# Optimization experiments

Measured on AMD Instinct MI355X. Metric: run time of the kernel, lower is better.

## Reference

```python
import jax, jax.numpy as jnp
import numpy as np

P, D, NF, NR, ND, EF, ER = 512, 128, 50000, 50000, 100000, 400000, 400000
BASELINE = 6.0


def setup_inputs() -> dict:
    key = jax.random.key(0)
    ctr = [0]
    def nk():
        ctr[0] += 1
        return jax.random.fold_in(key, ctr[0])
    def nrm(shape, scale=1.0):
        return jax.random.normal(nk(), shape, dtype=jnp.float32) * scale
    def uni(shape):
        return jax.random.uniform(nk(), shape, dtype=jnp.float32)
    def lin(fi, fo):
        return nrm((fi, fo), fi ** -0.5), jnp.zeros((fo,), jnp.float32)
    inp = {}
    inp['target_features'] = nrm((P,))
    inp['form_features'] = nrm((NF, P))
    inp['role_features'] = nrm((NR, P))
    inp['form_binds_y'] = BASELINE + nrm((EF,))
    inp['form_binds_w'] = uni((EF,))
    inp['role_binds_y'] = BASELINE + nrm((ER,))
    inp['role_binds_w'] = uni((ER,))
    inp['form_diff_w'] = uni((NF,)) + 0.01
    inp['role_diff_w'] = uni((NR,)) + 0.01
    inp['trust_vector'] = uni((3,))
    inp['drug_features'] = nrm((ND, D))
    inp['form_w1'], inp['form_b1'] = lin(P, P); inp['form_a1'] = jnp.full((1,), 0.25, jnp.float32)
    inp['form_w2'], inp['form_b2'] = lin(P, P)
    inp['role_w1'], inp['role_b1'] = lin(P, P); inp['role_a1'] = jnp.full((1,), 0.25, jnp.float32)
    inp['role_w2'], inp['role_b2'] = lin(P, P)
    inp['q_w'], inp['q_b'] = lin(P, D)
    inp['k_w'], inp['k_b'] = lin(D, D)
    inp['v_w'], inp['v_b'] = lin(D, D)
    inp['layer_emb'] = nrm((2, 16))
    inp['attn_w1'], inp['attn_b1'] = lin(2 * P + 16, 128)
    inp['attn_w2'], inp['attn_b2'] = lin(128, 64)
    inp['attn_w3'], inp['attn_b3'] = lin(64, 1)
    inp['mix_w1'], inp['mix_b1'] = lin(2 * D + 3, 64); inp['mix_a'] = jnp.full((1,), 0.25, jnp.float32)
    inp['mix_w2'], inp['mix_b2'] = lin(64, 2)
    inp['int_w1'], inp['int_b1'] = lin(D, P); inp['int_a'] = jnp.full((1,), 0.25, jnp.float32)
    inp['int_w2'], inp['int_b2'] = lin(P, P)
    inp['norm_w'] = jnp.ones((P,), jnp.float32)
    inp['norm_b'] = jnp.zeros((P,), jnp.float32)
    inp['delta_gate'] = jnp.float32(0.5)
    inp['form_neighbors'] = jnp.arange(NF, dtype=jnp.int32)
    inp['role_neighbors'] = jnp.arange(NR, dtype=jnp.int32)
    inp['form_binds_src'] = jax.random.randint(nk(), (EF,), 0, NF, dtype=jnp.int32)
    inp['form_binds_dst'] = jax.random.randint(nk(), (EF,), 0, ND, dtype=jnp.int32)
    inp['role_binds_src'] = jax.random.randint(nk(), (ER,), 0, NR, dtype=jnp.int32)
    inp['role_binds_dst'] = jax.random.randint(nk(), (ER,), 0, ND, dtype=jnp.int32)
    return inp


def _prelu(x, a):
    return jnp.where(x >= 0, x, a * x)


def _mlp2(x, w1, b1, a, w2, b2):
    return _prelu(x @ w1 + b1, a) @ w2 + b2


def _ln(x, w=None, b=None, eps=1e-5):
    m = jnp.mean(x, -1, keepdims=True)
    v = jnp.mean((x - m) ** 2, -1, keepdims=True)
    y = (x - m) * jax.lax.rsqrt(v + eps)
    return y if w is None else y * w + b


def _pref(z, nid, src, dst, y, w, drugs, q_w, q_b, k_w, k_b, v_w, v_b):
    # segment-softmax attention over (neighbor protein -> drug) bipartite edges
    N = nid.shape[0]
    order = jnp.argsort(nid)
    s = nid[order]
    pos = jnp.searchsorted(s, src)
    clip = jnp.minimum(pos, N - 1)
    valid = (pos < N) & (s[clip] == src)
    seg = jnp.where(valid, order[clip], N)  # invalid edges -> dump segment N
    q = z @ q_w + q_b                       # [D]
    d = drugs[dst]                          # [E, D] gather
    k = d @ k_w + k_b
    v = (d @ v_w + v_b) * ((y - BASELINE) * w)[:, None]
    logits = (k @ q) / (k.shape[-1] ** 0.5)
    mx = jax.ops.segment_max(logits, seg, num_segments=N + 1)
    mx = jnp.where(jnp.isfinite(mx), mx, 0.0)
    ex = jnp.where(valid, jnp.exp(logits - mx[seg]), 0.0)
    den = jax.ops.segment_sum(ex, seg, num_segments=N + 1) + 1e-12
    attn = ex / den[seg]
    return jax.ops.segment_sum(v * attn[:, None], seg, num_segments=N + 1)[:N]


def _attn_logits(z, zn, lemb, w1, b1, w2, b2, w3, b3):
    N = zn.shape[0]
    x = jnp.concatenate([jnp.broadcast_to(z, (N, z.shape[0])), zn,
                         jnp.broadcast_to(lemb, (N, lemb.shape[0]))], axis=-1)
    h = jax.nn.leaky_relu(x @ w1 + b1, 0.2)
    h = jax.nn.leaky_relu(h @ w2 + b2, 0.2)
    return (h @ w3 + b3)[:, 0]


def _core(fl, form_neighbors, role_neighbors, form_binds_src, form_binds_dst, role_binds_src, role_binds_dst):
    (target_features, form_features, role_features, form_binds_y, form_binds_w,
     role_binds_y, role_binds_w, form_diff_w, role_diff_w, trust_vector, drug_features,
     form_w1, form_b1, form_a1, form_w2, form_b2,
     role_w1, role_b1, role_a1, role_w2, role_b2,
     q_w, q_b, k_w, k_b, v_w, v_b, layer_emb,
     attn_w1, attn_b1, attn_w2, attn_b2, attn_w3, attn_b3,
     mix_w1, mix_b1, mix_a, mix_w2, mix_b2,
     int_w1, int_b1, int_a, int_w2, int_b2,
     norm_w, norm_b, delta_gate) = fl
    z_form = _mlp2(target_features, form_w1, form_b1, form_a1, form_w2, form_b2)
    z_role = _mlp2(target_features, role_w1, role_b1, role_a1, role_w2, role_b2)
    z = 0.5 * (z_form + z_role)
    form_feats = _mlp2(form_features, form_w1, form_b1, form_a1, form_w2, form_b2)
    role_feats = _mlp2(role_features, role_w1, role_b1, role_a1, role_w2, role_b2)
    form_msgs = _pref(z, form_neighbors, form_binds_src, form_binds_dst, form_binds_y, form_binds_w, drug_features, q_w, q_b, k_w, k_b, v_w, v_b)
    role_msgs = _pref(z, role_neighbors, role_binds_src, role_binds_dst, role_binds_y, role_binds_w, drug_features, q_w, q_b, k_w, k_b, v_w, v_b)
    form_logits = _attn_logits(z, form_feats, layer_emb[0], attn_w1, attn_b1, attn_w2, attn_b2, attn_w3, attn_b3)
    role_logits = _attn_logits(z, role_feats, layer_emb[1], attn_w1, attn_b1, attn_w2, attn_b2, attn_w3, attn_b3)
    form_attn = jax.nn.softmax(form_logits + jnp.log(jnp.maximum(form_diff_w, 1e-12)))
    role_attn = jax.nn.softmax(role_logits + jnp.log(jnp.maximum(role_diff_w, 1e-12)))
    v_form = form_attn @ form_msgs
    v_role = role_attn @ role_msgs
    mixer_in = jnp.concatenate([v_form, v_role, trust_vector])
    lw = jax.nn.softmax(_mlp2(mixer_in, mix_w1, mix_b1, mix_a, mix_w2, mix_b2))
    w_form, w_role = lw[0], lw[1]
    v_prior = w_form * v_form + w_role * v_role
    form_delta = form_attn @ (z[None, :] - form_feats)
    role_delta = role_attn @ (z[None, :] - role_feats)
    delta_raw = w_form * form_delta + w_role * role_delta
    delta_mean = delta_gate * _ln(delta_raw)
    z_refined = _ln(z + _mlp2(v_prior, int_w1, int_b1, int_a, int_w2, int_b2), norm_w, norm_b)
    return z_refined, v_prior, delta_mean


def reference(target_features, form_features, role_features, form_binds_y, form_binds_w, role_binds_y, role_binds_w, form_diff_w, role_diff_w, trust_vector, drug_features, form_w1, form_b1, form_a1, form_w2, form_b2, role_w1, role_b1, role_a1, role_w2, role_b2, q_w, q_b, k_w, k_b, v_w, v_b, layer_emb, attn_w1, attn_b1, attn_w2, attn_b2, attn_w3, attn_b3, mix_w1, mix_b1, mix_a, mix_w2, mix_b2, int_w1, int_b1, int_a, int_w2, int_b2, norm_w, norm_b, delta_gate, form_neighbors, role_neighbors, form_binds_src, form_binds_dst, role_binds_src, role_binds_dst):
    fl = (target_features, form_features, role_features, form_binds_y, form_binds_w,
          role_binds_y, role_binds_w, form_diff_w, role_diff_w, trust_vector, drug_features,
          form_w1, form_b1, form_a1, form_w2, form_b2,
          role_w1, role_b1, role_a1, role_w2, role_b2,
          q_w, q_b, k_w, k_b, v_w, v_b, layer_emb,
          attn_w1, attn_b1, attn_w2, attn_b2, attn_w3, attn_b3,
          mix_w1, mix_b1, mix_a, mix_w2, mix_b2,
          int_w1, int_b1, int_a, int_w2, int_b2,
          norm_w, norm_b, delta_gate)
    return _core(fl, form_neighbors, role_neighbors, form_binds_src, form_binds_dst, role_binds_src, role_binds_dst)
```

## Files before the change

kernel.cpp:

```cpp
#include <hip/hip_runtime.h>

#define NFN 50000
#define NDR 100000
#define NE  400000

__device__ __forceinline__ float bf2f(unsigned short u) {
    return __uint_as_float(((unsigned)u) << 16);
}
__device__ __forceinline__ unsigned short f2bf(float f) {
    unsigned u = __float_as_uint(f);
    unsigned r = 0x7FFFu + ((u >> 16) & 1u);
    return (unsigned short)((u + r) >> 16);
}

typedef __attribute__((ext_vector_type(8))) short bf16x8;
typedef __attribute__((ext_vector_type(4))) float f32x4;

struct KArgs {
    const float *tf, *ff, *rf, *fby, *fbw, *rby, *rbw, *fdw, *rdw, *trust, *drugs;
    const float *fw1, *fb1, *fa1, *fw2, *fb2, *rw1, *rb1, *ra1, *rw2, *rb2;
    const float *qw, *qb, *kw, *kb, *vw, *vb, *lemb;
    const float *aw1, *ab1, *aw2, *ab2, *aw3, *ab3;
    const float *mw1, *mb1, *ma, *mw2, *mb2;
    const float *iw1, *ib1, *ia, *iw2, *ib2;
    const float *nw, *nb, *dgate;
    const int *fsrc, *fdst, *rsrc, *rdst;
    float *shf, *shr;
    float *svf, *svr;
    float *gdenf, *gdenr;
    float *edenf, *edenr;
    float *cdf, *cdr;
    float *hraw;
    float *zraw;
    float *qraw;
    float *b1f, *b1r;
    float *sfr;
    float *o2raw;
    float *qk, *c0, *pe;
    unsigned short *w1tf, *w1tr;
    unsigned short *w2atf, *w2atr;
    unsigned short *aw2t;
    float *nexf, *nexr;
    unsigned short *H;
    unsigned short *Xb;
    float *hi;
    float *wfwr;
    float *out;
};

__global__ __launch_bounds__(512) void kA(KArgs A) {
    const int b = blockIdx.x;
    const int side = b >> 5, chunk = b & 31;
    const int tt = threadIdx.x;
    const float* w1 = side ? A.rw1 : A.fw1;
    float acc = 0.f;
    const int i0 = chunk * 16;
#pragma unroll
    for (int k = 0; k < 16; k++) {
        int i = i0 + k;
        acc = fmaf(A.tf[i], w1[(size_t)i * 512 + tt], acc);
    }
    atomicAdd(&A.hraw[side * 512 + tt], acc);
}

__global__ __launch_bounds__(512) void kB(KArgs A) {
    const int b = blockIdx.x;
    const int side = b >> 4, chunk = b & 15;
    const int tt = threadIdx.x;
    const float* w2 = side ? A.rw2 : A.fw2;
    const float* b1 = side ? A.rb1 : A.fb1;
    const float aa = (side ? A.ra1 : A.fa1)[0];
    float acc = 0.f;
    const int i0 = chunk * 32;
    for (int k = 0; k < 32; k++) {
        int i = i0 + k;
        float h = A.hraw[side * 512 + i] + b1[i];
        h = h >= 0.f ? h : aa * h;
        acc = fmaf(h, w2[(size_t)i * 512 + tt], acc);
    }
    if (b == 0) acc += A.fb2[tt] + A.rb2[tt];
    atomicAdd(&A.zraw[tt], acc);
}

__global__ __launch_bounds__(512) void kC1(KArgs A) {
    const int b = blockIdx.x;
    const int t = threadIdx.x;
    const int j = t & 127, isub = t >> 7;
    if (b < 8) {
        const int i0 = b * 64 + isub * 16;
        float acc = 0.f;
        for (int k = 0; k < 16; k++) {
            int i = i0 + k;
            acc = fmaf(0.5f * A.zraw[i], A.qw[(size_t)i * 128 + j], acc);
        }
        atomicAdd(&A.qraw[j], acc);
        if (b == 0 && t < 128) atomicAdd(&A.qraw[t], A.qb[t]);
    } else if (b < 16) {
        const int chunk = b - 8;
        const int i0 = chunk * 64 + isub * 16;
        float acc = 0.f;
        for (int k = 0; k < 16; k++) {
            int i = i0 + k;
            acc = fmaf(0.5f * A.zraw[i], A.aw1[(size_t)i * 128 + j], acc);
            acc = fmaf(A.fb2[i], A.aw1[(size_t)(512 + i) * 128 + j], acc);
        }
        atomicAdd(&A.b1f[j], acc);
        if (b == 8 && t < 128) {
            float c = A.ab1[t];
            for (int l = 0; l < 16; l++) c = fmaf(A.lemb[l], A.aw1[(size_t)(1024 + l) * 128 + t], c);
            atomicAdd(&A.b1f[t], c);
        }
    } else {
        const int chunk = b - 16;
        const int i0 = chunk * 64 + isub * 16;
        float acc = 0.f;
        for (int k = 0; k < 16; k++) {
            int i = i0 + k;
            acc = fmaf(0.5f * A.zraw[i], A.aw1[(size_t)i * 128 + j], acc);
            acc = fmaf(A.rb2[i], A.aw1[(size_t)(512 + i) * 128 + j], acc);
        }
        atomicAdd(&A.b1r[j], acc);
        if (b == 16 && t < 128) {
            float c = A.ab1[t];
            for (int l = 0; l < 16; l++) c = fmaf(A.lemb[16 + l], A.aw1[(size_t)(1024 + l) * 128 + t], c);
            atomicAdd(&A.b1r[t], c);
        }
    }
}

__global__ __launch_bounds__(256) void kC2(KArgs A) {
    const int t = threadIdx.x;
    __shared__ float sq[128];
    if (t < 128) sq[t] = A.qraw[t];
    __syncthreads();
    if (t < 128) {
        float s = 0.f;
        for (int j = 0; j < 128; j++) s = fmaf(A.kw[t * 128 + j], sq[j], s);
        A.qk[t] = s;
    } else if (t == 128) {
        float c = 0.f;
        for (int j = 0; j < 128; j++) c = fmaf(A.kb[j], sq[j], c);
        A.c0[0] = c;
    }
}

__global__ __launch_bounds__(256) void k_cvtX(const float* __restrict__ in,
                                              unsigned short* __restrict__ out, int n4) {
    int idx = blockIdx.x * 256 + threadIdx.x;
    const int stride = gridDim.x * 256;
    for (; idx < n4; idx += stride) {
        float4 v = ((const float4*)in)[idx];
        uint2 o;
        o.x = (unsigned)f2bf(v.x) | ((unsigned)f2bf(v.y) << 16);
        o.y = (unsigned)f2bf(v.z) | ((unsigned)f2bf(v.w) << 16);
        ((uint2*)out)[idx] = o;
    }
}

__global__ __launch_bounds__(512) void k_cvtW(KArgs A) {
    const int side = blockIdx.x >> 9;
    const int k = blockIdx.x & 511;
    const int n = threadIdx.x;
    const float* w1 = side ? A.rw1 : A.fw1;
    unsigned short* o = side ? A.w1tr : A.w1tf;
    o[(size_t)n * 512 + k] = f2bf(w1[k * 512 + n]);
}

__global__ __launch_bounds__(128) void k_cvtA2(KArgs A) {
    const int j = blockIdx.x;
    const int i = threadIdx.x;
    A.aw2t[j * 128 + i] = f2bf(A.aw2[i * 64 + j]);
}

__global__ __launch_bounds__(128) void k_w2a(KArgs A) {
    const int side = blockIdx.x >> 9;
    const int i = blockIdx.x & 511;
    const int j = threadIdx.x;
    const float* w2 = side ? A.rw2 : A.fw2;
    unsigned short* outp = side ? A.w2atr : A.w2atf;
    float s = 0.f;
    for (int k = 0; k < 512; k++)
        s = fmaf(w2[i * 512 + k], A.aw1[(size_t)(512 + k) * 128 + j], s);
    outp[(size_t)j * 512 + i] = f2bf(s);
}

__global__ __launch_bounds__(256, 2)
void mfma_gemm(const unsigned short* __restrict__ Ab, const unsigned short* __restrict__ Bt,
               const float* __restrict__ bias, const float* __restrict__ actp,
               unsigned short* __restrict__ Cv, int M, int N, int K, int NT) {
    __shared__ __align__(16) unsigned short Abuf[2][128 * 32];
    __shared__ __align__(16) unsigned short Bbuf[2][128 * 32];
    const int t = threadIdx.x;
    const int lane = t & 63, wv = t >> 6;
    int bid = blockIdx.x;
    if (NT > 1) {
        const int nwg = gridDim.x;
        const int q = nwg >> 3, r = nwg & 7;
        const int xcd = bid & 7, lx = bid >> 3;
        bid = (xcd < r ? xcd * (q + 1) : r * (q + 1) + (xcd - r) * q) + lx;
    }
    const int m0 = (bid / NT) * 128, n0 = (bid % NT) * 128;
    const int wm = (wv >> 1) * 64, wn = (wv & 1) * 64;
    const int lm = lane & 15, ko = lane >> 4;

    f32x4 acc[4][4];
#pragma unroll
    for (int i = 0; i < 4; i++)
#pragma unroll
        for (int j = 0; j < 4; j++) acc[i][j] = (f32x4){0.f, 0.f, 0.f, 0.f};

    const int nk = K >> 5;

    auto stage = [&](int buf, int k0) {
#pragma unroll
        for (int ii = 0; ii < 2; ii++) {
            const int inst = wv * 2 + ii;
            const int rl = inst * 16 + (lane >> 2);
            const int sl = (lane & 3) ^ ((rl >> 1) & 3);
            int ar = m0 + rl; if (ar >= M) ar = M - 1;
            __builtin_amdgcn_global_load_lds(
                (const __attribute__((address_space(1))) void*)(Ab + (size_t)ar * K + k0 + sl * 8),
                (__attribute__((address_space(3))) void*)(&Abuf[buf][inst * 512]), 16, 0, 0);
            __builtin_amdgcn_global_load_lds(
                (const __attribute__((address_space(1))) void*)(Bt + (size_t)(n0 + rl) * K + k0 + sl * 8),
                (__attribute__((address_space(3))) void*)(&Bbuf[buf][inst * 512]), 16, 0, 0);
        }
    };

    auto compute = [&](int buf) {
        bf16x8 af[4], bfr[4];
#pragma unroll
        for (int mi = 0; mi < 4; mi++) {
            int row = wm + mi * 16 + lm;
            af[mi] = *(const bf16x8*)&Abuf[buf][row * 32 + ((ko ^ ((row >> 1) & 3)) * 8)];
        }
#pragma unroll
        for (int ni = 0; ni < 4; ni++) {
            int col = wn + ni * 16 + lm;
            bfr[ni] = *(const bf16x8*)&Bbuf[buf][col * 32 + ((ko ^ ((col >> 1) & 3)) * 8)];
        }
#pragma unroll
        for (int mi = 0; mi < 4; mi++)
#pragma unroll
            for (int ni = 0; ni < 4; ni++)
                acc[mi][ni] = __builtin_amdgcn_mfma_f32_16x16x32_bf16(af[mi], bfr[ni], acc[mi][ni], 0, 0, 0);
    };

    stage(0, 0);
    __syncthreads();
    for (int kt = 0; kt < nk; kt++) {
        if (kt + 1 < nk) stage((kt + 1) & 1, (kt + 1) * 32);
        compute(kt & 1);
        __syncthreads();
    }

    const float aval = actp[0];
#pragma unroll
    for (int mi = 0; mi < 4; mi++) {
#pragma unroll
        for (int reg = 0; reg < 4; reg++) {
            int row = m0 + wm + mi * 16 + ko * 4 + reg;
            if (row >= M) continue;
#pragma unroll
            for (int ni = 0; ni < 4; ni++) {
                int col = n0 + wn + ni * 16 + lm;
                float v = acc[mi][ni][reg] + bias[col];
                v = v >= 0.f ? v : aval * v;
                Cv[(size_t)row * N + col] = f2bf(v);
            }
        }
    }
}

__global__ __launch_bounds__(256, 2)
void gemm_logits(KArgs A, int side) {
    __shared__ __align__(16) unsigned short Abuf[2][128 * 32];
    __shared__ __align__(16) unsigned short Bbuf[2][128 * 32];
    __shared__ __align__(16) unsigned short Gs[128][136];
    __shared__ float ps[128];
    const unsigned short* __restrict__ Ab = A.H;
    const unsigned short* __restrict__ Bt = side ? A.w2atr : A.w2atf;
    const float* __restrict__ bias = side ? A.b1r : A.b1f;
    const float* __restrict__ dw = side ? A.rdw : A.fdw;
    float* __restrict__ nex = side ? A.nexr : A.nexf;
    const int t = threadIdx.x;
    const int lane = t & 63, wv = t >> 6;
    const int m0 = blockIdx.x * 128;
    const int wm = (wv >> 1) * 64, wn = (wv & 1) * 64;
    const int lm = lane & 15, ko = lane >> 4;
    const int M = NFN, K = 512;

    f32x4 acc[4][4];
#pragma unroll
    for (int i = 0; i < 4; i++)
#pragma unroll
        for (int j = 0; j < 4; j++) acc[i][j] = (f32x4){0.f, 0.f, 0.f, 0.f};

    auto stage = [&](int buf, int k0) {
#pragma unroll
        for (int ii = 0; ii < 2; ii++) {
            const int inst = wv * 2 + ii;
            const int rl = inst * 16 + (lane >> 2);
            const int sl = (lane & 3) ^ ((rl >> 1) & 3);
            int ar = m0 + rl; if (ar >= M) ar = M - 1;
            __builtin_amdgcn_global_load_lds(
                (const __attribute__((address_space(1))) void*)(Ab + (size_t)ar * K + k0 + sl * 8),
                (__attribute__((address_space(3))) void*)(&Abuf[buf][inst * 512]), 16, 0, 0);
            __builtin_amdgcn_global_load_lds(
                (const __attribute__((address_space(1))) void*)(Bt + (size_t)rl * K + k0 + sl * 8),
                (__attribute__((address_space(3))) void*)(&Bbuf[buf][inst * 512]), 16, 0, 0);
        }
    };

    auto compute = [&](int buf) {
        bf16x8 af[4], bfr[4];
#pragma unroll
        for (int mi = 0; mi < 4; mi++) {
            int row = wm + mi * 16 + lm;
            af[mi] = *(const bf16x8*)&Abuf[buf][row * 32 + ((ko ^ ((row >> 1) & 3)) * 8)];
        }
#pragma unroll
        for (int ni = 0; ni < 4; ni++) {
            int col = wn + ni * 16 + lm;
            bfr[ni] = *(const bf16x8*)&Bbuf[buf][col * 32 + ((ko ^ ((col >> 1) & 3)) * 8)];
        }
#pragma unroll
        for (int mi = 0; mi < 4; mi++)
#pragma unroll
            for (int ni = 0; ni < 4; ni++)
                acc[mi][ni] = __builtin_amdgcn_mfma_f32_16x16x32_bf16(af[mi], bfr[ni], acc[mi][ni], 0, 0, 0);
    };

    stage(0, 0);
    __syncthreads();
    for (int kt = 0; kt < 16; kt++) {
        if (kt + 1 < 16) stage((kt + 1) & 1, (kt + 1) * 32);
        compute(kt & 1);
        __syncthreads();
    }

#pragma unroll
    for (int mi = 0; mi < 4; mi++) {
#pragma unroll
        for (int reg = 0; reg < 4; reg++) {
            int row_l = wm + mi * 16 + ko * 4 + reg;
#pragma unroll
            for (int ni = 0; ni < 4; ni++) {
                int col = wn + ni * 16 + lm;
                float v = acc[mi][ni][reg] + bias[col];
                v = v >= 0.f ? v : 0.2f * v;
                Gs[row_l][col] = f2bf(v);
            }
        }
    }
    __syncthreads();

    const int wr0 = wv * 32;
    float ab2v[4], aw3v[4];
#pragma unroll
    for (int ni = 0; ni < 4; ni++) {
        int col = ni * 16 + lm;
        ab2v[ni] = A.ab2[col];
        aw3v[ni] = A.aw3[col];
    }
    f32x4 acc2[2][4];
#pragma unroll
    for (int i = 0; i < 2; i++)
#pragma unroll
        for (int j = 0; j < 4; j++) acc2[i][j] = (f32x4){0.f, 0.f, 0.f, 0.f};
#pragma unroll
    for (int kk = 0; kk < 4; kk++) {
        bf16x8 ga[2], bb[4];
#pragma unroll
        for (int mi = 0; mi < 2; mi++)
            ga[mi] = *(const bf16x8*)&Gs[wr0 + mi * 16 + lm][kk * 32 + ko * 8];
#pragma unroll
        for (int ni = 0; ni < 4; ni++)
            bb[ni] = *(const bf16x8*)(A.aw2t + (size_t)(ni * 16 + lm) * 128 + kk * 32 + ko * 8);
#pragma unroll
        for (int mi = 0; mi < 2; mi++)
#pragma unroll
            for (int ni = 0; ni < 4; ni++)
                acc2[mi][ni] = __builtin_amdgcn_mfma_f32_16x16x32_bf16(ga[mi], bb[ni], acc2[mi][ni], 0, 0, 0);
    }
#pragma unroll
    for (int mi = 0; mi < 2; mi++) {
#pragma unroll
        for (int reg = 0; reg < 4; reg++) {
            float s = 0.f;
#pragma unroll
            for (int ni = 0; ni < 4; ni++) {
                float v = acc2[mi][ni][reg] + ab2v[ni];
                v = v >= 0.f ? v : 0.2f * v;
                s = fmaf(v, aw3v[ni], s);
            }
            s += __shfl_xor(s, 1, 64);
            s += __shfl_xor(s, 2, 64);
            s += __shfl_xor(s, 4, 64);
            s += __shfl_xor(s, 8, 64);
            if (lm == 0) ps[wr0 + mi * 16 + ko * 4 + reg] = s;
        }
    }
    __syncthreads();
    if (t < 128) {
        int node = m0 + t;
        if (node < M)
            nex[node] = expf(ps[t] + A.ab3[0] + logf(fmaxf(dw[node], 1e-12f)));
    }
}

__global__ __launch_bounds__(256) void k_nsum(KArgs A) {
    const int side = blockIdx.y;
    const float* nex = side ? A.nexr : A.nexf;
    float* gden = side ? A.gdenr : A.gdenf;
    float s = 0.f;
    for (int n = blockIdx.x * 256 + threadIdx.x; n < NFN; n += gridDim.x * 256)
        s += nex[n];
    __shared__ float red[256];
    red[threadIdx.x] = s; __syncthreads();
    for (int ss = 128; ss >= 1; ss >>= 1) {
        if (threadIdx.x < ss) red[threadIdx.x] += red[threadIdx.x + ss];
        __syncthreads();
    }
    if (threadIdx.x == 0) atomicAdd(gden, red[0]);
}

__global__ __launch_bounds__(256) void k_wsumH(KArgs A) {
    const int side = blockIdx.y;
    const int t = threadIdx.x;
    const int sub = t >> 6, colb = (t & 63) * 8;
    const float* nex = side ? A.nexr : A.nexf;
    const float invden = 1.0f / *(side ? A.gdenr : A.gdenf);
    float* SH = side ? A.shr : A.shf;
    float acc[8];
#pragma unroll
    for (int c = 0; c < 8; c++) acc[c] = 0.f;
    for (int rp = blockIdx.x; rp < NFN / 4; rp += gridDim.x) {
        const int row = rp * 4 + sub;
        const float a = nex[row] * invden;
        uint4 v = *(const uint4*)(A.H + (size_t)row * 512 + colb);
        unsigned vv[4] = {v.x, v.y, v.z, v.w};
#pragma unroll
        for (int u = 0; u < 4; u++) {
            acc[2 * u + 0] = fmaf(a, bf2f((unsigned short)(vv[u] & 0xFFFFu)), acc[2 * u + 0]);
            acc[2 * u + 1] = fmaf(a, bf2f((unsigned short)(vv[u] >> 16)), acc[2 * u + 1]);
        }
    }
    __shared__ float red[4][512];
#pragma unroll
    for (int c = 0; c < 8; c++) red[sub][colb + c] = acc[c];
    __syncthreads();
#pragma unroll
    for (int h = 0; h < 2; h++) {
        const int col = t + h * 256;
        atomicAdd(&SH[col], red[0][col] + red[1][col] + red[2][col] + red[3][col]);
    }
}

__global__ __launch_bounds__(256) void k_pd(KArgs A) {
    const int lane = threadIdx.x & 63;
    const int gw = blockIdx.x * 4 + (threadIdx.x >> 6);
    const int nw = gridDim.x * 4;
    const float2 qk2 = *(const float2*)(A.qk + 2 * lane);
    const float c0 = A.c0[0];
    for (int dr = gw; dr < NDR; dr += nw) {
        float2 dv = *(const float2*)(A.drugs + (size_t)dr * 128 + 2 * lane);
        float p = fmaf(dv.x, qk2.x, dv.y * qk2.y);
        for (int off = 32; off >= 1; off >>= 1) p += __shfl_xor(p, off, 64);
        if (lane == 0) A.pe[dr] = expf((p + c0) * 0.088388347648318447f);
    }
}

__global__ __launch_bounds__(256) void k_edge1(KArgs A) {
    const int side = blockIdx.y;
    const int* src = side ? A.rsrc : A.fsrc;
    const int* dst = side ? A.rdst : A.fdst;
    float* eden = side ? A.edenr : A.edenf;
    const int base = blockIdx.x * 1024 + threadIdx.x;
#pragma unroll
    for (int u = 0; u < 4; u++) {
        const int e = base + u * 256;
        if (e < NE) atomicAdd(&eden[src[e]], A.pe[dst[e]]);
    }
}

__global__ __launch_bounds__(256) void k_nfac(KArgs A) {
    const int side = blockIdx.y;
    const int n = blockIdx.x * 256 + threadIdx.x;
    if (n >= NFN) return;
    const float* nex = side ? A.nexr : A.nexf;
    float* eden = side ? A.edenr : A.edenf;
    const float invden = 1.0f / *(side ? A.gdenr : A.gdenf);
    eden[n] = nex[n] * invden / (eden[n] + 1e-12f);
}

__global__ __launch_bounds__(256) void k_edge2(KArgs A) {
    const int side = blockIdx.y;
    const int* src = side ? A.rsrc : A.fsrc;
    const int* dst = side ? A.rdst : A.fdst;
    const float* yy = side ? A.rby : A.fby;
    const float* ww = side ? A.rbw : A.fbw;
    const float* fac = side ? A.edenr : A.edenf;
    float* cd = side ? A.cdr : A.cdf;
    float* sv = side ? A.svr : A.svf;
    const int base = blockIdx.x * 1024 + threadIdx.x;
    float csum = 0.f;
#pragma unroll
    for (int u = 0; u < 4; u++) {
        const int e = base + u * 256;
        if (e < NE) {
            float coef = fac[src[e]] * A.pe[dst[e]] * ((yy[e] - 6.0f) * ww[e]);
            atomicAdd(&cd[dst[e]], coef);
            csum += coef;
        }
    }
    __shared__ float red[256];
    red[threadIdx.x] = csum; __syncthreads();
    for (int s2 = 128; s2 >= 1; s2 >>= 1) {
        if (threadIdx.x < s2) red[threadIdx.x] += red[threadIdx.x + s2];
        __syncthreads();
    }
    if (threadIdx.x == 0) atomicAdd(&sv[128], red[0]);
}

__global__ __launch_bounds__(256) void k_wsumD(KArgs A) {
    const int t = threadIdx.x;
    const int col = t & 127, rg = t >> 7;
    __shared__ float red[2][2][128];
    float af = 0.f, ar = 0.f;
    for (int dr = blockIdx.x * 2 + rg; dr < NDR; dr += gridDim.x * 2) {
        float cf = A.cdf[dr], cr = A.cdr[dr];
        float dv = A.drugs[(size_t)dr * 128 + col];
        af = fmaf(cf, dv, af);
        ar = fmaf(cr, dv, ar);
    }
    red[rg][0][col] = af; red[rg][1][col] = ar;
    __syncthreads();
    if (rg == 0) {
        atomicAdd(&A.svf[col], red[0][0][col] + red[1][0][col]);
        atomicAdd(&A.svr[col], red[0][1][col] + red[1][1][col]);
    }
}

__global__ __launch_bounds__(512) void kF1(KArgs A) {
    const int b = blockIdx.x;
    const int side = b >> 3, chunk = b & 7;
    const int tt = threadIdx.x;
    const float* w2 = side ? A.rw2 : A.fw2;
    const float* SH = side ? A.shr : A.shf;
    float acc = 0.f;
    const int i0 = chunk * 64;
    for (int k = 0; k < 64; k++) {
        int i = i0 + k;
        acc = fmaf(SH[i], w2[(size_t)i * 512 + tt], acc);
    }
    if (chunk == 0) acc += (side ? A.rb2 : A.fb2)[tt];
    atomicAdd(&A.sfr[side * 512 + tt], acc);
}

__global__ __launch_bounds__(512) void kF2(KArgs A) {
    const int t = threadIdx.x;
    __shared__ float vform[128], vrole[128], vprior[128], mh[64], sw[2];
    if (t < 128) {
        float vf = A.svf[128] * A.vb[t];
        float vr = A.svr[128] * A.vb[t];
        for (int i = 0; i < 128; i++) {
            vf = fmaf(A.svf[i], A.vw[i * 128 + t], vf);
            vr = fmaf(A.svr[i], A.vw[i * 128 + t], vr);
        }
        vform[t] = vf; vrole[t] = vr;
    }
    __syncthreads();
    if (t < 64) {
        float m = A.mb1[t];
        for (int i = 0; i < 128; i++) m = fmaf(vform[i], A.mw1[i * 64 + t], m);
        for (int i = 0; i < 128; i++) m = fmaf(vrole[i], A.mw1[(128 + i) * 64 + t], m);
        for (int i = 0; i < 3; i++)   m = fmaf(A.trust[i], A.mw1[(256 + i) * 64 + t], m);
        float ma = A.ma[0];
        mh[t] = m >= 0.f ? m : ma * m;
    }
    __syncthreads();
    if (t < 2) {
        float o = A.mb2[t];
        for (int i = 0; i < 64; i++) o = fmaf(mh[i], A.mw2[i * 2 + t], o);
        sw[t] = o;
    }
    __syncthreads();
    const float mo = fmaxf(sw[0], sw[1]);
    const float e0 = expf(sw[0] - mo), e1 = expf(sw[1] - mo);
    const float wf = e0 / (e0 + e1), wr = e1 / (e0 + e1);
    if (t == 0) { A.wfwr[0] = wf; A.wfwr[1] = wr; }
    if (t < 128) {
        float vp = wf * vform[t] + wr * vrole[t];
        vprior[t] = vp;
        A.out[512 + t] = vp;
    }
    __syncthreads();
    float hi = A.ib1[t];
    for (int i = 0; i < 128; i++) hi = fmaf(vprior[i], A.iw1[(size_t)i * 512 + t], hi);
    float ia = A.ia[0];
    A.hi[t] = hi >= 0.f ? hi : ia * hi;
}

__global__ __launch_bounds__(512) void kF3(KArgs A) {
    const int chunk = blockIdx.x;
    const int tt = threadIdx.x;
    float acc = 0.f;
    const int i0 = chunk * 64;
    for (int k = 0; k < 64; k++) {
        int i = i0 + k;
        acc = fmaf(A.hi[i], A.iw2[(size_t)i * 512 + tt], acc);
    }
    if (chunk == 0) acc += A.ib2[tt];
    atomicAdd(&A.o2raw[tt], acc);
}

__global__ __launch_bounds__(512) void kF4(KArgs A) {
    const int t = threadIdx.x;
    __shared__ float red[512];
    const float wf = A.wfwr[0], wr = A.wfwr[1];
    const float zv = 0.5f * A.zraw[t];
    float dr_ = zv - wf * A.sfr[t] - wr * A.sfr[512 + t];
    red[t] = dr_; __syncthreads();
    for (int s = 256; s >= 1; s >>= 1) { if (t < s) red[t] += red[t + s]; __syncthreads(); }
    float mean = red[0] * (1.f / 512.f); __syncthreads();
    float dd = dr_ - mean;
    red[t] = dd * dd; __syncthreads();
    for (int s = 256; s >= 1; s >>= 1) { if (t < s) red[t] += red[t + s]; __syncthreads(); }
    float var = red[0] * (1.f / 512.f); __syncthreads();
    A.out[640 + t] = A.dgate[0] * (dd * rsqrtf(var + 1e-5f));
    float zin = zv + A.o2raw[t];
    red[t] = zin; __syncthreads();
    for (int s = 256; s >= 1; s >>= 1) { if (t < s) red[t] += red[t + s]; __syncthreads(); }
    float mean2 = red[0] * (1.f / 512.f); __syncthreads();
    float d2 = zin - mean2;
    red[t] = d2 * d2; __syncthreads();
    for (int s = 256; s >= 1; s >>= 1) { if (t < s) red[t] += red[t + s]; __syncthreads(); }
    float var2 = red[0] * (1.f / 512.f);
    A.out[t] = (d2 * rsqrtf(var2 + 1e-5f)) * A.nw[t] + A.nb[t];
}

extern "C" void kernel_launch(void* const* d_in, const int* in_sizes, int n_in,
                              void* d_out, int out_size, void* d_ws, size_t ws_size,
                              hipStream_t stream) {
    (void)in_sizes; (void)n_in; (void)out_size;
    KArgs A;
    A.tf    = (const float*)d_in[0];
    A.ff    = (const float*)d_in[1];
    A.rf    = (const float*)d_in[2];
    A.fby   = (const float*)d_in[3];
    A.fbw   = (const float*)d_in[4];
    A.rby   = (const float*)d_in[5];
    A.rbw   = (const float*)d_in[6];
    A.fdw   = (const float*)d_in[7];
    A.rdw   = (const float*)d_in[8];
    A.trust = (const float*)d_in[9];
    A.drugs = (const float*)d_in[10];
    A.fw1 = (const float*)d_in[11]; A.fb1 = (const float*)d_in[12]; A.fa1 = (const float*)d_in[13];
    A.fw2 = (const float*)d_in[14]; A.fb2 = (const float*)d_in[15];
    A.rw1 = (const float*)d_in[16]; A.rb1 = (const float*)d_in[17]; A.ra1 = (const float*)d_in[18];
    A.rw2 = (const float*)d_in[19]; A.rb2 = (const float*)d_in[20];
    A.qw = (const float*)d_in[21]; A.qb = (const float*)d_in[22];
    A.kw = (const float*)d_in[23]; A.kb = (const float*)d_in[24];
    A.vw = (const float*)d_in[25]; A.vb = (const float*)d_in[26];
    A.lemb = (const float*)d_in[27];
    A.aw1 = (const float*)d_in[28]; A.ab1 = (const float*)d_in[29];
    A.aw2 = (const float*)d_in[30]; A.ab2 = (const float*)d_in[31];
    A.aw3 = (const float*)d_in[32]; A.ab3 = (const float*)d_in[33];
    A.mw1 = (const float*)d_in[34]; A.mb1 = (const float*)d_in[35]; A.ma = (const float*)d_in[36];
    A.mw2 = (const float*)d_in[37]; A.mb2 = (const float*)d_in[38];
    A.iw1 = (const float*)d_in[39]; A.ib1 = (const float*)d_in[40]; A.ia = (const float*)d_in[41];
    A.iw2 = (const float*)d_in[42]; A.ib2 = (const float*)d_in[43];
    A.nw = (const float*)d_in[44]; A.nb = (const float*)d_in[45];
    A.dgate = (const float*)d_in[46];
    A.fsrc = (const int*)d_in[49];
    A.fdst = (const int*)d_in[50];
    A.rsrc = (const int*)d_in[51];
    A.rdst = (const int*)d_in[52];
    A.out = (float*)d_out;

    char* w = (char*)d_ws;
    size_t off = 0;
    auto alloc = [&](size_t bytes) -> void* {
        void* p = w + off;
        off = (off + bytes + 255) & ~(size_t)255;
        return p;
    };
    A.shf   = (float*)alloc(512 * 4);
    A.shr   = (float*)alloc(512 * 4);
    A.svf   = (float*)alloc(129 * 4);
    A.svr   = (float*)alloc(129 * 4);
    A.gdenf = (float*)alloc(4);
    A.gdenr = (float*)alloc(4);
    A.edenf = (float*)alloc((size_t)NFN * 4);
    A.edenr = (float*)alloc((size_t)NFN * 4);
    A.cdf   = (float*)alloc((size_t)NDR * 4);
    A.cdr   = (float*)alloc((size_t)NDR * 4);
    A.hraw  = (float*)alloc(1024 * 4);
    A.zraw  = (float*)alloc(512 * 4);
    A.qraw  = (float*)alloc(128 * 4);
    A.b1f   = (float*)alloc(128 * 4);
    A.b1r   = (float*)alloc(128 * 4);
    A.sfr   = (float*)alloc(1024 * 4);
    A.o2raw = (float*)alloc(512 * 4);
    const size_t zbytes = off;
    A.qk   = (float*)alloc(128 * 4);
    A.c0   = (float*)alloc(4);
    A.pe   = (float*)alloc((size_t)NDR * 4);
    A.w1tf = (unsigned short*)alloc((size_t)512 * 512 * 2);
    A.w1tr = (unsigned short*)alloc((size_t)512 * 512 * 2);
    A.w2atf = (unsigned short*)alloc((size_t)128 * 512 * 2);
    A.w2atr = (unsigned short*)alloc((size_t)128 * 512 * 2);
    A.aw2t  = (unsigned short*)alloc((size_t)64 * 128 * 2);
    A.nexf  = (float*)alloc((size_t)NFN * 4);
    A.nexr  = (float*)alloc((size_t)NFN * 4);
    A.H     = (unsigned short*)alloc((size_t)NFN * 512 * 2);
    A.Xb    = (unsigned short*)alloc((size_t)NFN * 512 * 2);
    A.hi    = (float*)alloc(512 * 4);
    A.wfwr  = (float*)alloc(2 * 4);
    if (ws_size && off > ws_size) return;

    hipMemsetAsync(d_ws, 0, zbytes, stream);

    kA<<<64, 512, 0, stream>>>(A);
    kB<<<32, 512, 0, stream>>>(A);
    kC1<<<24, 512, 0, stream>>>(A);
    kC2<<<1, 256, 0, stream>>>(A);
    k_cvtW<<<1024, 512, 0, stream>>>(A);
    k_cvtA2<<<64, 128, 0, stream>>>(A);
    k_w2a<<<1024, 128, 0, stream>>>(A);
    k_pd<<<1024, 256, 0, stream>>>(A);

    const int MT = (NFN + 127) / 128;
    const int EB4 = (NE + 1023) / 1024;
    const int NFB = (NFN + 255) / 256;
    const int XN4 = NFN * 512 / 4;
    for (int side = 0; side < 2; side++) {
        const float* X  = side ? A.rf  : A.ff;
        const unsigned short* W1T = side ? A.w1tr : A.w1tf;
        const float* B1 = side ? A.rb1 : A.fb1;
        const float* A1 = side ? A.ra1 : A.fa1;
        k_cvtX<<<2048, 256, 0, stream>>>(X, A.Xb, XN4);
        mfma_gemm<<<MT * 4, 256, 0, stream>>>(A.Xb, W1T, B1, A1, A.H, NFN, 512, 512, 4);
        gemm_logits<<<MT, 256, 0, stream>>>(A, side);
    }
    k_nsum<<<dim3(64, 2), 256, 0, stream>>>(A);
    k_wsumH<<<dim3(1024, 2), 256, 0, stream>>>(A);
    k_edge1<<<dim3(EB4, 2), 256, 0, stream>>>(A);
    k_nfac<<<dim3(NFB, 2), 256, 0, stream>>>(A);
    k_edge2<<<dim3(EB4, 2), 256, 0, stream>>>(A);
    k_wsumD<<<512, 256, 0, stream>>>(A);
    kF1<<<16, 512, 0, stream>>>(A);
    kF2<<<1, 512, 0, stream>>>(A);
    kF3<<<8, 512, 0, stream>>>(A);
    kF4<<<1, 512, 0, stream>>>(A);
}
```

Before: 469.0 us.

## Batch form and role branches into single launches and fuse denominator sum

The per-side loop of conversion, first-layer GEMM and logits kernels is replaced by one launch of each kernel covering both sides, with padded per-side X and H buffers. The XCD-aware block remapping is rewritten for the combined grid. The separate k_nsum reduction is folded into gemm_logits as a block reduction plus atomic add. This removes several kernel launches and serialization points, and gives the small logits kernel a fuller grid, at the cost of doubled intermediate buffer memory. Giving each side its own H also means k_wsumH now reads that side's activations instead of whichever side wrote H last.

```diff
diff --git a/kernel.cpp b/kernel.cpp
--- a/kernel.cpp
+++ b/kernel.cpp
@@ -3,6 +3,8 @@
 #define NFN 50000
 #define NDR 100000
 #define NE  400000
+#define MT  391
+#define M0PAD 50048
 
 __device__ __forceinline__ float bf2f(unsigned short u) {
     return __uint_as_float(((unsigned)u) << 16);
@@ -144,16 +146,19 @@
     }
 }
 
-__global__ __launch_bounds__(256) void k_cvtX(const float* __restrict__ in,
-                                              unsigned short* __restrict__ out, int n4) {
+__global__ __launch_bounds__(256) void k_cvtX2(KArgs A) {
+    const int XN4 = NFN * 512 / 4;
+    const int P4 = M0PAD * 512 / 4;
     int idx = blockIdx.x * 256 + threadIdx.x;
     const int stride = gridDim.x * 256;
-    for (; idx < n4; idx += stride) {
-        float4 v = ((const float4*)in)[idx];
+    for (; idx < 2 * XN4; idx += stride) {
+        const int side = idx >= XN4;
+        const int li = idx - side * XN4;
+        float4 v = ((const float4*)(side ? A.rf : A.ff))[li];
         uint2 o;
         o.x = (unsigned)f2bf(v.x) | ((unsigned)f2bf(v.y) << 16);
         o.y = (unsigned)f2bf(v.z) | ((unsigned)f2bf(v.w) << 16);
-        ((uint2*)out)[idx] = o;
+        ((uint2*)A.Xb)[(size_t)side * P4 + li] = o;
     }
 }
 
@@ -185,31 +190,30 @@
 }
 
 __global__ __launch_bounds__(256, 2)
-void mfma_gemm(const unsigned short* __restrict__ Ab, const unsigned short* __restrict__ Bt,
-               const float* __restrict__ bias, const float* __restrict__ actp,
-               unsigned short* __restrict__ Cv, int M, int N, int K, int NT) {
+void mfma_gemm(KArgs A) {
     __shared__ __align__(16) unsigned short Abuf[2][128 * 32];
     __shared__ __align__(16) unsigned short Bbuf[2][128 * 32];
     const int t = threadIdx.x;
     const int lane = t & 63, wv = t >> 6;
-    int bid = blockIdx.x;
-    if (NT > 1) {
-        const int nwg = gridDim.x;
-        const int q = nwg >> 3, r = nwg & 7;
-        const int xcd = bid & 7, lx = bid >> 3;
-        bid = (xcd < r ? xcd * (q + 1) : r * (q + 1) + (xcd - r) * q) + lx;
-    }
-    const int m0 = (bid / NT) * 128, n0 = (bid % NT) * 128;
+    const int p = blockIdx.x;
+    const int L = (p & 7) * MT + (p >> 3);
+    const int side = L >= (MT * 4);
+    const int lbid = L - side * (MT * 4);
+    const int m0l = (lbid >> 2) * 128, n0 = (lbid & 3) * 128;
+    const unsigned short* __restrict__ Ab = A.Xb + (size_t)side * M0PAD * 512;
+    const unsigned short* __restrict__ Bt = side ? A.w1tr : A.w1tf;
+    const float* __restrict__ bias = side ? A.rb1 : A.fb1;
+    const float aval = (side ? A.ra1 : A.fa1)[0];
+    unsigned short* __restrict__ Cv = A.H + (size_t)side * M0PAD * 512;
     const int wm = (wv >> 1) * 64, wn = (wv & 1) * 64;
     const int lm = lane & 15, ko = lane >> 4;
+    const int K = 512;
 
     f32x4 acc[4][4];
 #pragma unroll
     for (int i = 0; i < 4; i++)
 #pragma unroll
         for (int j = 0; j < 4; j++) acc[i][j] = (f32x4){0.f, 0.f, 0.f, 0.f};
-
-    const int nk = K >> 5;
 
     auto stage = [&](int buf, int k0) {
 #pragma unroll
@@ -217,7 +221,7 @@
             const int inst = wv * 2 + ii;
             const int rl = inst * 16 + (lane >> 2);
             const int sl = (lane & 3) ^ ((rl >> 1) & 3);
-            int ar = m0 + rl; if (ar >= M) ar = M - 1;
+            int ar = m0l + rl; if (ar >= NFN) ar = NFN - 1;
             __builtin_amdgcn_global_load_lds(
                 (const __attribute__((address_space(1))) void*)(Ab + (size_t)ar * K + k0 + sl * 8),
                 (__attribute__((address_space(3))) void*)(&Abuf[buf][inst * 512]), 16, 0, 0);
@@ -248,47 +252,49 @@
 
     stage(0, 0);
     __syncthreads();
-    for (int kt = 0; kt < nk; kt++) {
-        if (kt + 1 < nk) stage((kt + 1) & 1, (kt + 1) * 32);
+    for (int kt = 0; kt < 16; kt++) {
+        if (kt + 1 < 16) stage((kt + 1) & 1, (kt + 1) * 32);
         compute(kt & 1);
         __syncthreads();
     }
 
-    const float aval = actp[0];
 #pragma unroll
     for (int mi = 0; mi < 4; mi++) {
 #pragma unroll
         for (int reg = 0; reg < 4; reg++) {
-            int row = m0 + wm + mi * 16 + ko * 4 + reg;
-            if (row >= M) continue;
+            int row = m0l + wm + mi * 16 + ko * 4 + reg;
 #pragma unroll
             for (int ni = 0; ni < 4; ni++) {
                 int col = n0 + wn + ni * 16 + lm;
                 float v = acc[mi][ni][reg] + bias[col];
                 v = v >= 0.f ? v : aval * v;
-                Cv[(size_t)row * N + col] = f2bf(v);
+                Cv[(size_t)row * 512 + col] = f2bf(v);
             }
         }
     }
 }
 
 __global__ __launch_bounds__(256, 2)
-void gemm_logits(KArgs A, int side) {
+void gemm_logits(KArgs A) {
     __shared__ __align__(16) unsigned short Abuf[2][128 * 32];
     __shared__ __align__(16) unsigned short Bbuf[2][128 * 32];
     __shared__ __align__(16) unsigned short Gs[128][136];
     __shared__ float ps[128];
-    const unsigned short* __restrict__ Ab = A.H;
+    __shared__ float red2[128];
+    const int bid = blockIdx.x;
+    const int side = bid >= MT;
+    const int m0l = (bid - side * MT) * 128;
+    const unsigned short* __restrict__ Ab = A.H + (size_t)side * M0PAD * 512;
     const unsigned short* __restrict__ Bt = side ? A.w2atr : A.w2atf;
     const float* __restrict__ bias = side ? A.b1r : A.b1f;
     const float* __restrict__ dw = side ? A.rdw : A.fdw;
     float* __restrict__ nex = side ? A.nexr : A.nexf;
+    float* __restrict__ gden = side ? A.gdenr : A.gdenf;
     const int t = threadIdx.x;
     const int lane = t & 63, wv = t >> 6;
-    const int m0 = blockIdx.x * 128;
     const int wm = (wv >> 1) * 64, wn = (wv & 1) * 64;
     const int lm = lane & 15, ko = lane >> 4;
-    const int M = NFN, K = 512;
+    const int K = 512;
 
     f32x4 acc[4][4];
 #pragma unroll
@@ -302,7 +308,7 @@
             const int inst = wv * 2 + ii;
             const int rl = inst * 16 + (lane >> 2);
             const int sl = (lane & 3) ^ ((rl >> 1) & 3);
-            int ar = m0 + rl; if (ar >= M) ar = M - 1;
+            int ar = m0l + rl; if (ar >= NFN) ar = NFN - 1;
             __builtin_amdgcn_global_load_lds(
                 (const __attribute__((address_space(1))) void*)(Ab + (size_t)ar * K + k0 + sl * 8),
                 (__attribute__((address_space(3))) void*)(&Abuf[buf][inst * 512]), 16, 0, 0);
@@ -402,27 +408,27 @@
         }
     }
     __syncthreads();
+    float val = 0.f;
     if (t < 128) {
-        int node = m0 + t;
-        if (node < M)
-            nex[node] = expf(ps[t] + A.ab3[0] + logf(fmaxf(dw[node], 1e-12f)));
-    }
-}
-
-__global__ __launch_bounds__(256) void k_nsum(KArgs A) {
-    const int side = blockIdx.y;
-    const float* nex = side ? A.nexr : A.nexf;
-    float* gden = side ? A.gdenr : A.gdenf;
-    float s = 0.f;
-    for (int n = blockIdx.x * 256 + threadIdx.x; n < NFN; n += gridDim.x * 256)
-        s += nex[n];
-    __shared__ float red[256];
-    red[threadIdx.x] = s; __syncthreads();
-    for (int ss = 128; ss >= 1; ss >>= 1) {
-        if (threadIdx.x < ss) red[threadIdx.x] += red[threadIdx.x + ss];
-        __syncthreads();
-    }
-    if (threadIdx.x == 0) atomicAdd(gden, red[0]);
+        int node = m0l + t;
+        if (node < NFN) {
+            val = expf(ps[t] + A.ab3[0] + logf(fmaxf(dw[node], 1e-12f)));
+            nex[node] = val;
+        }
+        red2[t] = val;
+    }
+    __syncthreads();
+    if (t < 64) red2[t] += red2[t + 64];
+    __syncthreads();
+    if (t < 32) red2[t] += red2[t + 32];
+    __syncthreads();
+    if (t < 16) red2[t] += red2[t + 16];
+    __syncthreads();
+    if (t == 0) {
+        float s = 0.f;
+        for (int i = 0; i < 16; i++) s += red2[i];
+        atomicAdd(gden, s);
+    }
 }
 
 __global__ __launch_bounds__(256) void k_wsumH(KArgs A) {
@@ -432,13 +438,14 @@
     const float* nex = side ? A.nexr : A.nexf;
     const float invden = 1.0f / *(side ? A.gdenr : A.gdenf);
     float* SH = side ? A.shr : A.shf;
+    const unsigned short* Hs = A.H + (size_t)side * M0PAD * 512;
     float acc[8];
 #pragma unroll
     for (int c = 0; c < 8; c++) acc[c] = 0.f;
     for (int rp = blockIdx.x; rp < NFN / 4; rp += gridDim.x) {
         const int row = rp * 4 + sub;
         const float a = nex[row] * invden;
-        uint4 v = *(const uint4*)(A.H + (size_t)row * 512 + colb);
+        uint4 v = *(const uint4*)(Hs + (size_t)row * 512 + colb);
         unsigned vv[4] = {v.x, v.y, v.z, v.w};
 #pragma unroll
         for (int u = 0; u < 4; u++) {
@@ -714,8 +721,8 @@
     A.aw2t  = (unsigned short*)alloc((size_t)64 * 128 * 2);
     A.nexf  = (float*)alloc((size_t)NFN * 4);
     A.nexr  = (float*)alloc((size_t)NFN * 4);
-    A.H     = (unsigned short*)alloc((size_t)NFN * 512 * 2);
-    A.Xb    = (unsigned short*)alloc((size_t)NFN * 512 * 2);
+    A.H     = (unsigned short*)alloc((size_t)2 * M0PAD * 512 * 2);
+    A.Xb    = (unsigned short*)alloc((size_t)2 * M0PAD * 512 * 2);
     A.hi    = (float*)alloc(512 * 4);
     A.wfwr  = (float*)alloc(2 * 4);
     if (ws_size && off > ws_size) return;
@@ -731,20 +738,11 @@
     k_w2a<<<1024, 128, 0, stream>>>(A);
     k_pd<<<1024, 256, 0, stream>>>(A);
 
-    const int MT = (NFN + 127) / 128;
     const int EB4 = (NE + 1023) / 1024;
     const int NFB = (NFN + 255) / 256;
-    const int XN4 = NFN * 512 / 4;
-    for (int side = 0; side < 2; side++) {
-        const float* X  = side ? A.rf  : A.ff;
-        const unsigned short* W1T = side ? A.w1tr : A.w1tf;
-        const float* B1 = side ? A.rb1 : A.fb1;
-        const float* A1 = side ? A.ra1 : A.fa1;
-        k_cvtX<<<2048, 256, 0, stream>>>(X, A.Xb, XN4);
-        mfma_gemm<<<MT * 4, 256, 0, stream>>>(A.Xb, W1T, B1, A1, A.H, NFN, 512, 512, 4);
-        gemm_logits<<<MT, 256, 0, stream>>>(A, side);
-    }
-    k_nsum<<<dim3(64, 2), 256, 0, stream>>>(A);
+    k_cvtX2<<<2048, 256, 0, stream>>>(A);
+    mfma_gemm<<<2 * MT * 4, 256, 0, stream>>>(A);
+    gemm_logits<<<2 * MT, 256, 0, stream>>>(A);
     k_wsumH<<<dim3(1024, 2), 256, 0, stream>>>(A);
     k_edge1<<<dim3(EB4, 2), 256, 0, stream>>>(A);
     k_nfac<<<dim3(NFB, 2), 256, 0, stream>>>(A);
```

New measurement: 494.7 us. 1.05x slower.
